# Kernel tuning notes

Measured on AMD Instinct MI355X. Metric: run time of the kernel, lower is better.

## Reference

```python
import jax, jax.numpy as jnp
import numpy as np

HIDDEN = 896
N_HEADS = 14
N_KV = 2
HEAD_DIM = 64
GROUPS = N_HEADS // N_KV  # 7
ROPE_THETA = 1000000.0
B, S = 2, 2048
NEG = -1e9


def rotate_half(x):
    x1 = x[..., : x.shape[-1] // 2]
    x2 = x[..., x.shape[-1] // 2:]
    return jnp.concatenate([-x2, x1], axis=-1)


def setup_inputs() -> dict:
    key = jax.random.key(0)
    ks = jax.random.split(key, 8)
    scale = 0.02
    hidden_states = jax.random.normal(ks[0], (B, S, HIDDEN), dtype=jnp.float32)
    # causal additive mask [1,1,S,S]
    causal = jnp.tril(jnp.ones((S, S), dtype=bool))
    attention_mask = jnp.where(causal, 0.0, NEG).astype(jnp.float32)[None, None]
    Wq = jax.random.normal(ks[1], (HIDDEN, N_HEADS * HEAD_DIM), dtype=jnp.float32) * scale
    bq = jnp.zeros((N_HEADS * HEAD_DIM,), dtype=jnp.float32)
    Wk = jax.random.normal(ks[2], (HIDDEN, N_KV * HEAD_DIM), dtype=jnp.float32) * scale
    bk = jnp.zeros((N_KV * HEAD_DIM,), dtype=jnp.float32)
    Wv = jax.random.normal(ks[3], (HIDDEN, N_KV * HEAD_DIM), dtype=jnp.float32) * scale
    bv = jnp.zeros((N_KV * HEAD_DIM,), dtype=jnp.float32)
    Wo = jax.random.normal(ks[4], (HIDDEN, HIDDEN), dtype=jnp.float32) * scale
    return {"hidden_states": hidden_states, "attention_mask": attention_mask,
            "Wq": Wq, "bq": bq, "Wk": Wk, "bk": bk, "Wv": Wv, "bv": bv,
            "Wo": Wo, "position_offset": 0}


def reference(hidden_states, attention_mask, Wq, bq, Wk, bk, Wv, bv, Wo, position_offset):
    batch, seq, _ = hidden_states.shape
    # QKV projections -> [B, heads, S, head_dim]
    q = (hidden_states @ Wq + bq).reshape(batch, seq, N_HEADS, HEAD_DIM).transpose(0, 2, 1, 3)
    k = (hidden_states @ Wk + bk).reshape(batch, seq, N_KV, HEAD_DIM).transpose(0, 2, 1, 3)
    v = (hidden_states @ Wv + bv).reshape(batch, seq, N_KV, HEAD_DIM).transpose(0, 2, 1, 3)
    # RoPE (computed inline from position_offset, matches precomputed cos/sin tables)
    inv_freq = 1.0 / (ROPE_THETA ** (jnp.arange(0, HEAD_DIM, 2, dtype=jnp.float32) / HEAD_DIM))
    pos = (position_offset + jnp.arange(seq)).astype(jnp.float32)  # [S]
    freqs = pos[:, None] * inv_freq[None, :]  # [S, HD/2]
    emb = jnp.concatenate([freqs, freqs], axis=-1)  # [S, HD]
    cos = jnp.cos(emb)[None, None]  # [1,1,S,HD]
    sin = jnp.sin(emb)[None, None]
    q = q * cos + rotate_half(q) * sin
    k = k * cos + rotate_half(k) * sin
    # GQA: repeat kv heads
    k = jnp.repeat(k, GROUPS, axis=1)
    v = jnp.repeat(v, GROUPS, axis=1)
    scores = jnp.einsum('bhqd,bhkd->bhqk', q, k) / jnp.sqrt(jnp.float32(HEAD_DIM))
    scores = scores + attention_mask
    weights = jax.nn.softmax(scores, axis=-1)
    out = jnp.einsum('bhqk,bhkd->bhqd', weights, v)
    out = out.transpose(0, 2, 1, 3).reshape(batch, seq, HIDDEN)
    return out @ Wo
```

## Files before the change

kernel.cpp:

```cpp
#include <hip/hip_runtime.h>
#include <stdint.h>

#define DEV __device__ __forceinline__

using bf16x8 = __attribute__((ext_vector_type(8))) short;
using f32x4  = __attribute__((ext_vector_type(4))) float;

DEV float b2f(uint16_t h){ return __uint_as_float(((uint32_t)h)<<16); }
DEV uint16_t f2b(float f){ uint32_t u=__float_as_uint(f); u += 0x7fffu + ((u>>16)&1u); return (uint16_t)(u>>16); }
DEV uint32_t pk2(float a, float b){
  return __builtin_amdgcn_perm(__float_as_uint(b), __float_as_uint(a), 0x07060302u);
}
DEV float fexp2(float x){ float r; asm("v_exp_f32 %0, %1" : "=v"(r) : "v"(x)); return r; }

#define GLOAD16(gp, lp) __builtin_amdgcn_global_load_lds( \
    (__attribute__((address_space(1))) void*)(gp), \
    (__attribute__((address_space(3))) void*)(lp), 16, 0, 0)

constexpr int S_    = 2048;
constexpr int HID   = 896;
constexpr int NH    = 14;
constexpr int NKV   = 2;
constexpr int HD    = 64;
constexpr int BATCH = 2;
constexpr int MROWS = BATCH * S_;
constexpr int NQKV  = 1152;
constexpr int SROWS = 1536;
constexpr int OPSTR = BATCH * NH * SROWS * 64;
constexpr int MLSTR = BATCH * NH * SROWS;
constexpr float QSCALE = 0.125f * 1.4426950408889634f;

__global__ void prep_all_kernel(const float* __restrict__ X,
                                const float* __restrict__ Wq, const float* __restrict__ Wk,
                                const float* __restrict__ Wv, const float* __restrict__ Wo,
                                const float* __restrict__ bq, const float* __restrict__ bk,
                                const float* __restrict__ bv, const int* __restrict__ pos0,
                                uint16_t* __restrict__ Xb,
                                uint16_t* __restrict__ WqkvT, uint16_t* __restrict__ WoT,
                                float* __restrict__ bqkv,
                                float* __restrict__ cosT, float* __restrict__ sinT) {
  const int blk = blockIdx.x, tid = threadIdx.x;
  if (blk < 1792) {
    const int lx = tid & 31, ly = tid >> 5;
    const float* src; uint16_t* dst; int ncols, rowOff, i;
    if (blk < 784)       { src = Wq; dst = WqkvT; ncols = 896; rowOff = 0;    i = blk;       }
    else if (blk < 896)  { src = Wk; dst = WqkvT; ncols = 128; rowOff = 896;  i = blk - 784; }
    else if (blk < 1008) { src = Wv; dst = WqkvT; ncols = 128; rowOff = 1024; i = blk - 896; }
    else                 { src = Wo; dst = WoT;   ncols = 896; rowOff = 0;    i = blk - 1008;}
    const int nb = ncols >> 5;
    const int n0 = (i % nb) * 32, k0 = (i / nb) * 32;
    __shared__ uint16_t tile[32][33];
    #pragma unroll
    for (int r = 0; r < 32; r += 8)
      tile[ly + r][lx] = f2b(src[(size_t)(k0 + ly + r) * ncols + (n0 + lx)]);
    __syncthreads();
    #pragma unroll
    for (int r = 0; r < 32; r += 8)
      dst[(size_t)(rowOff + n0 + ly + r) * 896 + (k0 + lx)] = tile[lx][ly + r];
  } else if (blk < 5376) {
    int i = (blk - 1792) * 256 + tid;
    float4 v = ((const float4*)X)[i];
    union { uint16_t u[4]; uint64_t q; } r;
    r.u[0] = f2b(v.x); r.u[1] = f2b(v.y); r.u[2] = f2b(v.z); r.u[3] = f2b(v.w);
    ((uint64_t*)Xb)[i] = r.q;
  } else if (blk < 5632) {
    int idx = (blk - 5376) * 256 + tid;
    int s = idx >> 5, j = idx & 31;
    float inv = exp2f(-(float)j * (19.931568569324174f / 32.0f));
    float ang = (float)(pos0[0] + s) * inv;
    float sv, cv;
    sincosf(ang, &sv, &cv);
    cosT[idx] = cv; sinT[idx] = sv;
  } else {
    int i = (blk - 5632) * 256 + tid;
    if (i < NQKV) bqkv[i] = i < 896 ? bq[i] : (i < 1024 ? bk[i - 896] : bv[i - 1024]);
  }
}

__global__ void packv_kernel(const uint16_t* __restrict__ Vf, uint16_t* __restrict__ Vt) {
  __shared__ uint16_t tile[64][65];
  const int s0 = blockIdx.x * 64;
  const int g  = blockIdx.y;
  const int b = g >> 1, kv = g & 1;
  const int lx = threadIdx.x & 63, ly = threadIdx.x >> 6;
  #pragma unroll
  for (int i = 0; i < 64; i += 4)
    tile[ly + i][lx] = Vf[(size_t)(b * S_ + s0 + ly + i) * 128 + kv * 64 + lx];
  __syncthreads();
  const int col = (lx & 32) | ((lx & 8) << 1) | ((lx & 4) << 1) | ((lx & 16) >> 2) | (lx & 3);
  #pragma unroll
  for (int i = 0; i < 64; i += 4)
    Vt[((size_t)g * HD + ly + i) * S_ + s0 + col] = tile[lx][ly + i];
}

template <int EPI>
__global__ __launch_bounds__(256) void gemm_bt_kernel(
    const uint16_t* __restrict__ A, const uint16_t* __restrict__ Bt,
    const float* __restrict__ bias, void* __restrict__ Cv, int N, int K,
    const float* __restrict__ cosT, const float* __restrict__ sinT,
    uint16_t* __restrict__ Qb, uint16_t* __restrict__ Kb, uint16_t* __restrict__ Vf) {
  __shared__ __align__(16) uint16_t As[2][128 * 64];
  __shared__ __align__(16) uint16_t Bs[2][64 * 64];
  const int tid = threadIdx.x;
  const int l = tid & 63, w = tid >> 6;
  const int m0 = blockIdx.x * 128, n0 = blockIdx.y * 64;
  const int wr = w * 32;

  auto stage = [&](int k0, int bi) {
    #pragma unroll
    for (int i = 0; i < 4; ++i) {
      int cid = i * 256 + tid;
      int row = cid >> 3;
      int sch = (cid & 7) ^ (row & 7);
      GLOAD16(A + (size_t)(m0 + row) * K + (k0 + sch * 8), (char*)As[bi] + cid * 16);
    }
    #pragma unroll
    for (int i = 0; i < 2; ++i) {
      int cid = i * 256 + tid;
      int row = cid >> 3;
      int sch = (cid & 7) ^ (row & 7);
      GLOAD16(Bt + (size_t)(n0 + row) * K + (k0 + sch * 8), (char*)Bs[bi] + cid * 16);
    }
  };

  const int nk = K >> 6;
  f32x4 acc[2][4] = {};
  stage(0, 0);
  asm volatile("s_waitcnt vmcnt(0)" ::: "memory");
  __builtin_amdgcn_s_barrier();

  #pragma unroll 1
  for (int t = 0; t < nk; ++t) {
    if (t + 1 < nk) stage((t + 1) << 6, (t + 1) & 1);
    const uint16_t* Ac = As[t & 1];
    const uint16_t* Bc = Bs[t & 1];
    __builtin_amdgcn_s_setprio(1);
    #pragma unroll
    for (int ks = 0; ks < 2; ++ks) {
      bf16x8 af[2], bfr[4];
      #pragma unroll
      for (int mi = 0; mi < 2; ++mi) {
        int row = wr + mi * 16 + (l & 15);
        int ch = ((l >> 4) + ks * 4) ^ (row & 7);
        af[mi] = *(const bf16x8*)((const char*)Ac + row * 128 + ch * 16);
      }
      #pragma unroll
      for (int ni = 0; ni < 4; ++ni) {
        int row = ni * 16 + (l & 15);
        int ch = ((l >> 4) + ks * 4) ^ (row & 7);
        bfr[ni] = *(const bf16x8*)((const char*)Bc + row * 128 + ch * 16);
      }
      #pragma unroll
      for (int mi = 0; mi < 2; ++mi)
        #pragma unroll
        for (int ni = 0; ni < 4; ++ni)
          acc[mi][ni] = __builtin_amdgcn_mfma_f32_16x16x32_bf16(af[mi], bfr[ni], acc[mi][ni], 0, 0, 0);
    }
    __builtin_amdgcn_s_setprio(0);
    asm volatile("s_waitcnt vmcnt(0)" ::: "memory");
    __builtin_amdgcn_s_barrier();
  }

  const int tc = l & 15, g = l >> 4;
  if (EPI == 1) {
    if (n0 < 896) {
      #pragma unroll
      for (int mi = 0; mi < 2; ++mi) {
        #pragma unroll
        for (int jr = 0; jr < 4; ++jr) {
          int row = m0 + wr + mi * 16 + g * 4 + jr;
          int bb = row >> 11, s = row & (S_ - 1);
          const float* cp = cosT + s * 32;
          const float* sp = sinT + s * 32;
          #pragma unroll
          for (int ni = 0; ni < 2; ++ni) {
            int col = n0 + ni * 16 + tc;
            int j = col & 63;
            float c = cp[j], sn = sp[j];
            float alo = acc[mi][ni][jr] + bias[col];
            float ahi = acc[mi][ni + 2][jr] + bias[col + 32];
            size_t dst = ((size_t)(bb * NH + (n0 >> 6)) * S_ + s) * HD + j;
            Qb[dst]      = f2b((alo * c - ahi * sn) * QSCALE);
            Qb[dst + 32] = f2b((ahi * c + alo * sn) * QSCALE);
          }
        }
      }
    } else if (n0 < 1024) {
      #pragma unroll
      for (int mi = 0; mi < 2; ++mi) {
        #pragma unroll
        for (int jr = 0; jr < 4; ++jr) {
          int row = m0 + wr + mi * 16 + g * 4 + jr;
          int bb = row >> 11, s = row & (S_ - 1);
          const float* cp = cosT + s * 32;
          const float* sp = sinT + s * 32;
          #pragma unroll
          for (int ni = 0; ni < 2; ++ni) {
            int col = n0 + ni * 16 + tc;
            int j = col & 63;
            float c = cp[j], sn = sp[j];
            float alo = acc[mi][ni][jr] + bias[col];
            float ahi = acc[mi][ni + 2][jr] + bias[col + 32];
            size_t dst = ((size_t)(bb * NKV + ((n0 - 896) >> 6)) * S_ + s) * HD + j;
            Kb[dst]      = f2b(alo * c - ahi * sn);
            Kb[dst + 32] = f2b(ahi * c + alo * sn);
          }
        }
      }
    } else {
      #pragma unroll
      for (int mi = 0; mi < 2; ++mi)
        #pragma unroll
        for (int ni = 0; ni < 4; ++ni) {
          int col = n0 + ni * 16 + tc;
          #pragma unroll
          for (int jr = 0; jr < 4; ++jr) {
            int row = m0 + wr + mi * 16 + g * 4 + jr;
            Vf[(size_t)row * 128 + (col - 1024)] = f2b(acc[mi][ni][jr] + bias[col]);
          }
        }
    }
  } else {
    #pragma unroll
    for (int mi = 0; mi < 2; ++mi) {
      #pragma unroll
      for (int ni = 0; ni < 4; ++ni) {
        int col = n0 + ni * 16 + tc;
        #pragma unroll
        for (int j = 0; j < 4; ++j) {
          int row = m0 + wr + mi * 16 + g * 4 + j;
          ((float*)Cv)[(size_t)row * N + col] = acc[mi][ni][j];
        }
      }
    }
  }
}

__global__ __launch_bounds__(448) void attn_kernel(
    const uint16_t* __restrict__ Qb, const uint16_t* __restrict__ Kb,
    const uint16_t* __restrict__ Vt, uint16_t* __restrict__ Ob,
    uint16_t* __restrict__ Op, float2* __restrict__ mlp) {
  __shared__ __align__(16) uint16_t Ks[2][64 * 64];
  __shared__ __align__(16) uint16_t Vs[2][64 * 64];
  const int tid = threadIdx.x, l = tid & 63, w = tid >> 6;
  const int u = blockIdx.x;
  const int kv = blockIdx.y & 1, b = blockIdx.y >> 1;
  const int tc = l & 15, g = l >> 4;

  int qt16, ck;
  if (u < 32)       { qt16 = u;                   ck = 0; }
  else if (u < 96)  { int i = u - 32;  qt16 = 32 + (i >> 1); ck = i & 1; }
  else if (u < 192) { int i = u - 96;  int q3 = i / 3; qt16 = 64 + q3; ck = i - 3 * q3; }
  else              { int i = u - 192; qt16 = 96 + (i >> 2); ck = i & 3; }
  const int ntiles = (qt16 >> 2) + 1;
  const int nch    = (qt16 >> 5) + 1;
  const int tlo    = 8 * ck;
  const int thi    = (8 * ck + 8 < ntiles) ? (8 * ck + 8) : ntiles;
  const int ns     = thi - tlo;
  const bool dodiag = (ck == nch - 1);
  const bool split  = (nch > 1);

  const int h  = kv * 7 + w;
  const int qg = qt16 * 16 + tc;

  const uint16_t* Khead = Kb + (size_t)(b * NKV + kv) * S_ * HD;
  const uint16_t* Vhead = Vt + (size_t)(b * NKV + kv) * HD * S_;

  auto stage = [&](int t, int bi) {
    const int t0 = t * 64;
    #pragma unroll
    for (int i = 0; i < 2; ++i) {
      if (i == 0 || tid < 64) {
        int cid = i * 448 + tid;
        int row = cid >> 3, sch = (cid & 7) ^ (row & 7);
        GLOAD16(Khead + (size_t)(t0 + row) * HD + sch * 8, (char*)Ks[bi] + cid * 16);
        GLOAD16(Vhead + (size_t)row * S_ + t0 + sch * 8,   (char*)Vs[bi] + cid * 16);
      }
    }
  };

  const uint16_t* qptr = Qb + ((size_t)(b * NH + h) * S_ + qg) * HD + g * 8;
  bf16x8 qf0 = *(const bf16x8*)qptr;
  bf16x8 qf1 = *(const bf16x8*)(qptr + 32);

  f32x4 oacc[4] = {};
  float mrow = -1e30f, lrow = 0.f;

  stage(tlo, 0);

  #pragma unroll 1
  for (int i = 0; i < ns; ++i) {
    const int t = tlo + i;
    asm volatile("s_waitcnt vmcnt(0)" ::: "memory");
    __builtin_amdgcn_s_barrier();
    if (i + 1 < ns) stage(t + 1, (i + 1) & 1);

    const uint16_t* Kc = Ks[i & 1];
    const uint16_t* Vc = Vs[i & 1];
    const int t0 = t * 64;

    f32x4 sacc[4] = {};
    __builtin_amdgcn_s_setprio(1);
    #pragma unroll
    for (int ks = 0; ks < 2; ++ks) {
      bf16x8 qf = ks ? qf1 : qf0;
      #pragma unroll
      for (int c = 0; c < 4; ++c) {
        int trow = c * 16 + tc;
        int ch = (g + ks * 4) ^ (tc & 7);
        bf16x8 kf = *(const bf16x8*)((const char*)Kc + trow * 128 + ch * 16);
        sacc[c] = __builtin_amdgcn_mfma_f32_16x16x32_bf16(kf, qf, sacc[c], 0, 0, 0);
      }
    }
    __builtin_amdgcn_s_setprio(0);

    if (dodiag && t == ntiles - 1) {
      #pragma unroll
      for (int c = 0; c < 4; ++c) {
        int kvb = t0 + c * 16 + g * 4;
        #pragma unroll
        for (int r = 0; r < 4; ++r)
          if (kvb + r > qg) sacc[c][r] = -1e30f;
      }
    }

    float pmax = sacc[0][0];
    #pragma unroll
    for (int c = 0; c < 4; ++c)
      #pragma unroll
      for (int r = 0; r < 4; ++r) pmax = fmaxf(pmax, sacc[c][r]);
    if (__any(pmax > mrow + 11.5f)) {
      float mt = fmaxf(pmax, __shfl_xor(pmax, 16));
      mt = fmaxf(mt, __shfl_xor(mt, 32));
      float mn = fmaxf(mrow, mt);
      float corr = fexp2(mrow - mn);
      mrow = mn;
      lrow *= corr;
      #pragma unroll
      for (int dt = 0; dt < 4; ++dt) oacc[dt] *= corr;
    }
    float rs = 0.f;
    #pragma unroll
    for (int c = 0; c < 4; ++c)
      #pragma unroll
      for (int r = 0; r < 4; ++r) {
        float e = fexp2(sacc[c][r] - mrow);
        sacc[c][r] = e; rs += e;
      }
    lrow += rs;

    uint32_t w0[4], w1[4];
    #pragma unroll
    for (int c = 0; c < 4; ++c) {
      w0[c] = pk2(sacc[c][0], sacc[c][1]);
      w1[c] = pk2(sacc[c][2], sacc[c][3]);
    }
    bf16x8 pf[2];
    {
      union { uint32_t u[4]; bf16x8 v; } p0, p1;
      p0.u[0] = w0[0]; p0.u[1] = w1[0]; p0.u[2] = w0[1]; p0.u[3] = w1[1];
      p1.u[0] = w0[2]; p1.u[1] = w1[2]; p1.u[2] = w0[3]; p1.u[3] = w1[3];
      pf[0] = p0.v; pf[1] = p1.v;
    }

    __builtin_amdgcn_s_setprio(1);
    #pragma unroll
    for (int ks = 0; ks < 2; ++ks) {
      #pragma unroll
      for (int dt = 0; dt < 4; ++dt) {
        int drow = dt * 16 + tc;
        int vch = (g + ks * 4) ^ (tc & 7);
        bf16x8 vf = *(const bf16x8*)((const char*)Vc + drow * 128 + vch * 16);
        oacc[dt] = __builtin_amdgcn_mfma_f32_16x16x32_bf16(vf, pf[ks], oacc[dt], 0, 0, 0);
      }
    }
    __builtin_amdgcn_s_setprio(0);
  }

  float ltot = lrow;
  ltot += __shfl_xor(ltot, 16);
  ltot += __shfl_xor(ltot, 32);

  if (!split) {
    float inv = 1.0f / ltot;
    size_t obase = (size_t)(b * S_ + qg) * HID + h * HD;
    #pragma unroll
    for (int dt = 0; dt < 4; ++dt) {
      union { uint16_t u[4]; uint64_t q; } o;
      #pragma unroll
      for (int r = 0; r < 4; ++r) o.u[r] = f2b(oacc[dt][r] * inv);
      *(uint64_t*)(Ob + obase + dt * 16 + g * 4) = o.q;
    }
  } else {
    size_t rowid = (size_t)(b * NH + h) * SROWS + (qg - 512);
    uint16_t* Opc = Op + (size_t)ck * OPSTR + rowid * 64;
    #pragma unroll
    for (int dt = 0; dt < 4; ++dt) {
      union { uint16_t u[4]; uint64_t q; } o;
      #pragma unroll
      for (int r = 0; r < 4; ++r) o.u[r] = f2b(oacc[dt][r]);
      *(uint64_t*)(Opc + dt * 16 + g * 4) = o.q;
    }
    if (g == 0) mlp[(size_t)ck * MLSTR + rowid] = make_float2(mrow, ltot);
  }
}

__global__ void combine_kernel(const uint16_t* __restrict__ Op, const float2* __restrict__ mlp,
                               uint16_t* __restrict__ Ob) {
  int idx = blockIdx.x * 256 + threadIdx.x;
  int r = idx >> 4;
  int d0 = (idx & 15) * 4;
  int bh = r / SROWS;
  int sr = r - bh * SROWS;
  int s = 512 + sr;
  int nch = (s >> 9) + 1;
  float M = -1e30f;
  #pragma unroll 4
  for (int c = 0; c < 4; ++c)
    if (c < nch) M = fmaxf(M, mlp[(size_t)c * MLSTR + r].x);
  float den = 0.f, acc[4] = {0.f, 0.f, 0.f, 0.f};
  #pragma unroll 4
  for (int c = 0; c < 4; ++c) {
    if (c >= nch) continue;
    float2 ml = mlp[(size_t)c * MLSTR + r];
    float wg = fexp2(ml.x - M);
    den += ml.y * wg;
    union { uint16_t u[4]; uint64_t q; } o;
    o.q = *(const uint64_t*)(Op + (size_t)c * OPSTR + (size_t)r * 64 + d0);
    #pragma unroll
    for (int j = 0; j < 4; ++j) acc[j] += b2f(o.u[j]) * wg;
  }
  float inv = 1.0f / den;
  union { uint16_t u[4]; uint64_t q; } oo;
  #pragma unroll
  for (int j = 0; j < 4; ++j) oo.u[j] = f2b(acc[j] * inv);
  int bb = bh / NH, hh = bh - bb * NH;
  *(uint64_t*)(Ob + (size_t)(bb * S_ + s) * HID + hh * HD + d0) = oo.q;
}

extern "C" void kernel_launch(void* const* d_in, const int* in_sizes, int n_in,
                              void* d_out, int out_size, void* d_ws, size_t ws_size,
                              hipStream_t stream) {
  (void)in_sizes; (void)n_in; (void)out_size; (void)ws_size;
  const float* X  = (const float*)d_in[0];
  const float* Wq = (const float*)d_in[2];
  const float* bq = (const float*)d_in[3];
  const float* Wk = (const float*)d_in[4];
  const float* bk = (const float*)d_in[5];
  const float* Wv = (const float*)d_in[6];
  const float* bv = (const float*)d_in[7];
  const float* Wo = (const float*)d_in[8];
  const int* pos  = (const int*)d_in[9];

  char* p = (char*)d_ws;
  auto carve = [&](size_t n) -> char* { char* r = p; p += (n + 255) & ~(size_t)255; return r; };

  uint16_t* Xb    = (uint16_t*)carve((size_t)MROWS * HID * 2);
  uint16_t* WqkvT = (uint16_t*)carve((size_t)NQKV * 896 * 2);
  uint16_t* WoT   = (uint16_t*)carve((size_t)896 * 896 * 2);
  float*    bqkv  = (float*)carve((size_t)NQKV * 4);
  float*    cosT  = (float*)carve((size_t)S_ * 32 * 4);
  float*    sinT  = (float*)carve((size_t)S_ * 32 * 4);
  uint16_t* Qb    = (uint16_t*)carve((size_t)MROWS * HID * 2);
  uint16_t* Kb    = (uint16_t*)carve((size_t)MROWS * 128 * 2);
  uint16_t* Vf    = (uint16_t*)carve((size_t)MROWS * 128 * 2);
  uint16_t* Vt    = (uint16_t*)carve((size_t)MROWS * 128 * 2);
  uint16_t* Op    = (uint16_t*)carve((size_t)OPSTR * 4 * 2);
  float2*   mlp   = (float2*)carve((size_t)MLSTR * 4 * 8);
  uint16_t* Ob    = Xb;

  prep_all_kernel<<<dim3(5637), 256, 0, stream>>>(X, Wq, Wk, Wv, Wo, bq, bk, bv, pos,
                                                  Xb, WqkvT, WoT, bqkv, cosT, sinT);

  gemm_bt_kernel<1><<<dim3(MROWS / 128, NQKV / 64), 256, 0, stream>>>(
      Xb, WqkvT, bqkv, nullptr, NQKV, 896, cosT, sinT, Qb, Kb, Vf);

  packv_kernel<<<dim3(S_ / 64, BATCH * NKV), 256, 0, stream>>>(Vf, Vt);

  attn_kernel<<<dim3(320, NKV * BATCH), 448, 0, stream>>>(Qb, Kb, Vt, Ob, Op, mlp);
  combine_kernel<<<dim3(BATCH * NH * SROWS * 16 / 256), 256, 0, stream>>>(Op, mlp, Ob);

  gemm_bt_kernel<0><<<dim3(MROWS / 128, 896 / 64), 256, 0, stream>>>(
      Ob, WoT, nullptr, d_out, 896, 896, nullptr, nullptr, nullptr, nullptr, nullptr);
}
```

Before: 87.37 us.

## Process two 16-row query tiles per wave to reuse staged K/V tiles

```diff
diff --git a/kernel.cpp b/kernel.cpp
--- a/kernel.cpp
+++ b/kernel.cpp
@@ -247,21 +247,22 @@
   const int kv = blockIdx.y & 1, b = blockIdx.y >> 1;
   const int tc = l & 15, g = l >> 4;
 
-  int qt16, ck;
-  if (u < 32)       { qt16 = u;                   ck = 0; }
-  else if (u < 96)  { int i = u - 32;  qt16 = 32 + (i >> 1); ck = i & 1; }
-  else if (u < 192) { int i = u - 96;  int q3 = i / 3; qt16 = 64 + q3; ck = i - 3 * q3; }
-  else              { int i = u - 192; qt16 = 96 + (i >> 2); ck = i & 3; }
-  const int ntiles = (qt16 >> 2) + 1;
-  const int nch    = (qt16 >> 5) + 1;
+  int q32, ck;
+  if (u < 16)      { q32 = u;                 ck = 0; }
+  else if (u < 48) { int i = u - 16; q32 = 16 + (i >> 1); ck = i & 1; }
+  else if (u < 96) { int i = u - 48; int q3 = i / 3; q32 = 32 + q3; ck = i - 3 * q3; }
+  else             { int i = u - 96; q32 = 48 + (i >> 2); ck = i & 3; }
+  const int ntiles = (q32 >> 1) + 1;
+  const int nch    = (ntiles + 7) >> 3;
   const int tlo    = 8 * ck;
-  const int thi    = (8 * ck + 8 < ntiles) ? (8 * ck + 8) : ntiles;
+  const int thi    = (tlo + 8 < ntiles) ? (tlo + 8) : ntiles;
   const int ns     = thi - tlo;
   const bool dodiag = (ck == nch - 1);
   const bool split  = (nch > 1);
 
-  const int h  = kv * 7 + w;
-  const int qg = qt16 * 16 + tc;
+  const int h   = kv * 7 + w;
+  const int qgA = q32 * 32 + tc;
+  const int qgB = qgA + 16;
 
   const uint16_t* Khead = Kb + (size_t)(b * NKV + kv) * S_ * HD;
   const uint16_t* Vhead = Vt + (size_t)(b * NKV + kv) * HD * S_;
@@ -279,12 +280,13 @@
     }
   };
 
-  const uint16_t* qptr = Qb + ((size_t)(b * NH + h) * S_ + qg) * HD + g * 8;
-  bf16x8 qf0 = *(const bf16x8*)qptr;
-  bf16x8 qf1 = *(const bf16x8*)(qptr + 32);
-
-  f32x4 oacc[4] = {};
-  float mrow = -1e30f, lrow = 0.f;
+  const uint16_t* qpA = Qb + ((size_t)(b * NH + h) * S_ + qgA) * HD + g * 8;
+  const uint16_t* qpB = qpA + (size_t)16 * HD;
+  bf16x8 qA0 = *(const bf16x8*)qpA, qA1 = *(const bf16x8*)(qpA + 32);
+  bf16x8 qB0 = *(const bf16x8*)qpB, qB1 = *(const bf16x8*)(qpB + 32);
+
+  f32x4 oA[4] = {}, oB[4] = {};
+  float mA = -1e30f, lA = 0.f, mB = -1e30f, lB = 0.f;
 
   stage(tlo, 0);
 
@@ -299,17 +301,19 @@
     const uint16_t* Vc = Vs[i & 1];
     const int t0 = t * 64;
 
-    f32x4 sacc[4] = {};
+    f32x4 sA[4] = {}, sB[4] = {};
     __builtin_amdgcn_s_setprio(1);
     #pragma unroll
     for (int ks = 0; ks < 2; ++ks) {
-      bf16x8 qf = ks ? qf1 : qf0;
+      bf16x8 qfA = ks ? qA1 : qA0;
+      bf16x8 qfB = ks ? qB1 : qB0;
       #pragma unroll
       for (int c = 0; c < 4; ++c) {
         int trow = c * 16 + tc;
         int ch = (g + ks * 4) ^ (tc & 7);
         bf16x8 kf = *(const bf16x8*)((const char*)Kc + trow * 128 + ch * 16);
-        sacc[c] = __builtin_amdgcn_mfma_f32_16x16x32_bf16(kf, qf, sacc[c], 0, 0, 0);
+        sA[c] = __builtin_amdgcn_mfma_f32_16x16x32_bf16(kf, qfA, sA[c], 0, 0, 0);
+        sB[c] = __builtin_amdgcn_mfma_f32_16x16x32_bf16(kf, qfB, sB[c], 0, 0, 0);
       }
     }
     __builtin_amdgcn_s_setprio(0);
@@ -319,48 +323,49 @@
       for (int c = 0; c < 4; ++c) {
         int kvb = t0 + c * 16 + g * 4;
         #pragma unroll
-        for (int r = 0; r < 4; ++r)
-          if (kvb + r > qg) sacc[c][r] = -1e30f;
-      }
-    }
-
-    float pmax = sacc[0][0];
+        for (int r = 0; r < 4; ++r) {
+          if (kvb + r > qgA) sA[c][r] = -1e30f;
+          if (kvb + r > qgB) sB[c][r] = -1e30f;
+        }
+      }
+    }
+
+    float pA = sA[0][0], pB = sB[0][0];
     #pragma unroll
     for (int c = 0; c < 4; ++c)
       #pragma unroll
-      for (int r = 0; r < 4; ++r) pmax = fmaxf(pmax, sacc[c][r]);
-    if (__any(pmax > mrow + 11.5f)) {
-      float mt = fmaxf(pmax, __shfl_xor(pmax, 16));
-      mt = fmaxf(mt, __shfl_xor(mt, 32));
-      float mn = fmaxf(mrow, mt);
-      float corr = fexp2(mrow - mn);
-      mrow = mn;
-      lrow *= corr;
-      #pragma unroll
-      for (int dt = 0; dt < 4; ++dt) oacc[dt] *= corr;
-    }
-    float rs = 0.f;
+      for (int r = 0; r < 4; ++r) { pA = fmaxf(pA, sA[c][r]); pB = fmaxf(pB, sB[c][r]); }
+    if (__any(fmaxf(pA - mA, pB - mB) > 11.5f)) {
+      float mtA = fmaxf(pA, __shfl_xor(pA, 16)); mtA = fmaxf(mtA, __shfl_xor(mtA, 32));
+      float mtB = fmaxf(pB, __shfl_xor(pB, 16)); mtB = fmaxf(mtB, __shfl_xor(mtB, 32));
+      float mnA = fmaxf(mA, mtA), mnB = fmaxf(mB, mtB);
+      float cA = fexp2(mA - mnA), cB = fexp2(mB - mnB);
+      mA = mnA; mB = mnB; lA *= cA; lB *= cB;
+      #pragma unroll
+      for (int dt = 0; dt < 4; ++dt) { oA[dt] *= cA; oB[dt] *= cB; }
+    }
+    float rsA = 0.f, rsB = 0.f;
     #pragma unroll
     for (int c = 0; c < 4; ++c)
       #pragma unroll
       for (int r = 0; r < 4; ++r) {
-        float e = fexp2(sacc[c][r] - mrow);
-        sacc[c][r] = e; rs += e;
-      }
-    lrow += rs;
-
-    uint32_t w0[4], w1[4];
-    #pragma unroll
-    for (int c = 0; c < 4; ++c) {
-      w0[c] = pk2(sacc[c][0], sacc[c][1]);
-      w1[c] = pk2(sacc[c][2], sacc[c][3]);
-    }
-    bf16x8 pf[2];
+        float eA = fexp2(sA[c][r] - mA); sA[c][r] = eA; rsA += eA;
+        float eB = fexp2(sB[c][r] - mB); sB[c][r] = eB; rsB += eB;
+      }
+    lA += rsA; lB += rsB;
+
+    bf16x8 pfA[2], pfB[2];
     {
-      union { uint32_t u[4]; bf16x8 v; } p0, p1;
-      p0.u[0] = w0[0]; p0.u[1] = w1[0]; p0.u[2] = w0[1]; p0.u[3] = w1[1];
-      p1.u[0] = w0[2]; p1.u[1] = w1[2]; p1.u[2] = w0[3]; p1.u[3] = w1[3];
-      pf[0] = p0.v; pf[1] = p1.v;
+      union { uint32_t u[4]; bf16x8 v; } t0A, t1A, t0B, t1B;
+      t0A.u[0] = pk2(sA[0][0], sA[0][1]); t0A.u[1] = pk2(sA[0][2], sA[0][3]);
+      t0A.u[2] = pk2(sA[1][0], sA[1][1]); t0A.u[3] = pk2(sA[1][2], sA[1][3]);
+      t1A.u[0] = pk2(sA[2][0], sA[2][1]); t1A.u[1] = pk2(sA[2][2], sA[2][3]);
+      t1A.u[2] = pk2(sA[3][0], sA[3][1]); t1A.u[3] = pk2(sA[3][2], sA[3][3]);
+      t0B.u[0] = pk2(sB[0][0], sB[0][1]); t0B.u[1] = pk2(sB[0][2], sB[0][3]);
+      t0B.u[2] = pk2(sB[1][0], sB[1][1]); t0B.u[3] = pk2(sB[1][2], sB[1][3]);
+      t1B.u[0] = pk2(sB[2][0], sB[2][1]); t1B.u[1] = pk2(sB[2][2], sB[2][3]);
+      t1B.u[2] = pk2(sB[3][0], sB[3][1]); t1B.u[3] = pk2(sB[3][2], sB[3][3]);
+      pfA[0] = t0A.v; pfA[1] = t1A.v; pfB[0] = t0B.v; pfB[1] = t1B.v;
     }
 
     __builtin_amdgcn_s_setprio(1);
@@ -371,37 +376,44 @@
         int drow = dt * 16 + tc;
         int vch = (g + ks * 4) ^ (tc & 7);
         bf16x8 vf = *(const bf16x8*)((const char*)Vc + drow * 128 + vch * 16);
-        oacc[dt] = __builtin_amdgcn_mfma_f32_16x16x32_bf16(vf, pf[ks], oacc[dt], 0, 0, 0);
+        oA[dt] = __builtin_amdgcn_mfma_f32_16x16x32_bf16(vf, pfA[ks], oA[dt], 0, 0, 0);
+        oB[dt] = __builtin_amdgcn_mfma_f32_16x16x32_bf16(vf, pfB[ks], oB[dt], 0, 0, 0);
       }
     }
     __builtin_amdgcn_s_setprio(0);
   }
 
-  float ltot = lrow;
-  ltot += __shfl_xor(ltot, 16);
-  ltot += __shfl_xor(ltot, 32);
+  float ltA = lA; ltA += __shfl_xor(ltA, 16); ltA += __shfl_xor(ltA, 32);
+  float ltB = lB; ltB += __shfl_xor(ltB, 16); ltB += __shfl_xor(ltB, 32);
 
   if (!split) {
-    float inv = 1.0f / ltot;
-    size_t obase = (size_t)(b * S_ + qg) * HID + h * HD;
+    float iA = 1.0f / ltA, iB = 1.0f / ltB;
+    size_t baseA = (size_t)(b * S_ + qgA) * HID + h * HD;
+    size_t baseB = (size_t)(b * S_ + qgB) * HID + h * HD;
     #pragma unroll
     for (int dt = 0; dt < 4; ++dt) {
-      union { uint16_t u[4]; uint64_t q; } o;
-      #pragma unroll
-      for (int r = 0; r < 4; ++r) o.u[r] = f2b(oacc[dt][r] * inv);
-      *(uint64_t*)(Ob + obase + dt * 16 + g * 4) = o.q;
+      union { uint16_t u[4]; uint64_t q; } a, bb_;
+      #pragma unroll
+      for (int r = 0; r < 4; ++r) { a.u[r] = f2b(oA[dt][r] * iA); bb_.u[r] = f2b(oB[dt][r] * iB); }
+      *(uint64_t*)(Ob + baseA + dt * 16 + g * 4) = a.q;
+      *(uint64_t*)(Ob + baseB + dt * 16 + g * 4) = bb_.q;
     }
   } else {
-    size_t rowid = (size_t)(b * NH + h) * SROWS + (qg - 512);
-    uint16_t* Opc = Op + (size_t)ck * OPSTR + rowid * 64;
+    size_t ridA = (size_t)(b * NH + h) * SROWS + (qgA - 512);
+    uint16_t* OpA = Op + (size_t)ck * OPSTR + ridA * 64;
+    uint16_t* OpB = OpA + (size_t)16 * 64;
     #pragma unroll
     for (int dt = 0; dt < 4; ++dt) {
-      union { uint16_t u[4]; uint64_t q; } o;
-      #pragma unroll
-      for (int r = 0; r < 4; ++r) o.u[r] = f2b(oacc[dt][r]);
-      *(uint64_t*)(Opc + dt * 16 + g * 4) = o.q;
-    }
-    if (g == 0) mlp[(size_t)ck * MLSTR + rowid] = make_float2(mrow, ltot);
+      union { uint16_t u[4]; uint64_t q; } a, bb_;
+      #pragma unroll
+      for (int r = 0; r < 4; ++r) { a.u[r] = f2b(oA[dt][r]); bb_.u[r] = f2b(oB[dt][r]); }
+      *(uint64_t*)(OpA + dt * 16 + g * 4) = a.q;
+      *(uint64_t*)(OpB + dt * 16 + g * 4) = bb_.q;
+    }
+    if (g == 0) {
+      mlp[(size_t)ck * MLSTR + ridA] = make_float2(mA, ltA);
+      mlp[(size_t)ck * MLSTR + ridA + 16] = make_float2(mB, ltB);
+    }
   }
 }
 
@@ -477,7 +489,7 @@
 
   packv_kernel<<<dim3(S_ / 64, BATCH * NKV), 256, 0, stream>>>(Vf, Vt);
 
-  attn_kernel<<<dim3(320, NKV * BATCH), 448, 0, stream>>>(Qb, Kb, Vt, Ob, Op, mlp);
+  attn_kernel<<<dim3(160, NKV * BATCH), 448, 0, stream>>>(Qb, Kb, Vt, Ob, Op, mlp);
   combine_kernel<<<dim3(BATCH * NH * SROWS * 16 / 256), 256, 0, stream>>>(Op, mlp, Ob);
 
   gemm_bt_kernel<0><<<dim3(MROWS / 128, 896 / 64), 256, 0, stream>>>(
```

After: 98.96 us. 1.13x slower.
